# Performance work log

Hardware: AMD Instinct MI355X
Metric: run time of the kernel (lower is better)

The kernel has to match this reference:

```python
import jax, jax.numpy as jnp
import numpy as np

KSIZE = 7
HEAD_DIM = 64
EPS = 1e-6

def rmsnorm(x, w):
    return x * jax.lax.rsqrt(jnp.mean(x * x, axis=-1, keepdims=True) + EPS) * w

def rope2d(x):
    # Split channels: first half rotated by row position, second half by column position.
    B, H, W, C = x.shape
    half = C // 2
    q = half // 2
    inv = 1.0 / (10000.0 ** (jnp.arange(q, dtype=jnp.float32) / q))
    th_y = jnp.arange(H, dtype=jnp.float32)[:, None] * inv  # [H,q]
    th_x = jnp.arange(W, dtype=jnp.float32)[:, None] * inv  # [W,q]
    def rot(v, th):  # v: [...,q,2], th broadcastable to [...,q]
        c, s = jnp.cos(th), jnp.sin(th)
        a, b = v[..., 0], v[..., 1]
        return jnp.stack([a * c - b * s, a * s + b * c], axis=-1)
    xy = rot(x[..., :half].reshape(B, H, W, q, 2), th_y[None, :, None, :])
    xx = rot(x[..., half:].reshape(B, H, W, q, 2), th_x[None, None, :, :])
    return jnp.concatenate([xy.reshape(B, H, W, half), xx.reshape(B, H, W, half)], axis=-1)

def neighborhood_attn(x, w_qkv, w_proj, b_proj, k=KSIZE, hd=HEAD_DIM):
    # NATTEN semantics: each query attends to a k x k window; window start is
    # clamped at borders so every query sees exactly k*k keys.
    B, H, W, C = x.shape
    nh = C // hd
    qkv = x @ w_qkv                           # [B,H,W,3C]
    qv, kv, vv = jnp.split(qkv, 3, axis=-1)
    qh = qv.reshape(B, H, W, nh, hd)
    kh = kv.reshape(B, H, W, nh, hd)
    vh = vv.reshape(B, H, W, nh, hd)
    idx_h = jnp.clip(jnp.arange(H) - k // 2, 0, H - k)[:, None] + jnp.arange(k)  # [H,k]
    idx_w = jnp.clip(jnp.arange(W) - k // 2, 0, W - k)[:, None] + jnp.arange(k)  # [W,k]
    def gather(t):  # [B,H,W,nh,hd] -> [B,H,W,nh,k*k,hd]
        g = t[:, idx_h]            # [B,H,k,W,nh,hd]
        g = g[:, :, :, idx_w]      # [B,H,k,W,k,nh,hd]
        return g.transpose(0, 1, 3, 5, 2, 4, 6).reshape(B, H, W, nh, k * k, hd)
    kn = gather(kh)
    vn = gather(vh)
    scale = 1.0 / np.sqrt(hd).astype(np.float32)
    logits = jnp.einsum('bxynd,bxynkd->bxynk', qh, kn) * scale
    attn = jax.nn.softmax(logits, axis=-1)
    out = jnp.einsum('bxynk,bxynkd->bxynd', attn, vn).reshape(B, H, W, C)
    return out @ w_proj + b_proj

def geglu(x, ff1_w, ff1_b, ff2_w, ff2_b):
    h = x @ ff1_w + ff1_b
    gate, value = jnp.split(h, 2, axis=-1)
    return (jax.nn.gelu(gate, approximate=False) * value) @ ff2_w + ff2_b

def setup_inputs():
    key = jax.random.key(0)
    B, H, W, C = 2, 64, 64, 256
    ks = jax.random.split(key, 8)
    g = lambda k, shape, sc: jax.random.normal(k, shape, jnp.float32) * sc
    return {
        'x': g(ks[0], (B, H, W, C), 1.0),
        'norm1_w': jnp.ones((C,), jnp.float32),
        'norm2_w': jnp.ones((C,), jnp.float32),
        'w_qkv': g(ks[1], (C, 3 * C), 0.02),
        'w_proj': g(ks[2], (C, C), 0.02),
        'b_proj': g(ks[3], (C,), 0.02),
        'ff1_w': g(ks[4], (C, 2 * C), 0.02),
        'ff1_b': g(ks[5], (2 * C,), 0.02),
        'ff2_w': g(ks[6], (C, C), 0.02),
        'ff2_b': g(ks[7], (C,), 0.02),
    }

def reference(x, norm1_w, norm2_w, w_qkv, w_proj, b_proj, ff1_w, ff1_b, ff2_w, ff2_b):
    h = rope2d(rmsnorm(x, norm1_w))
    x = x + neighborhood_attn(h, w_qkv, w_proj, b_proj)
    x = x + geglu(rmsnorm(x, norm2_w), ff1_w, ff1_b, ff2_w, ff2_b)
    return x
```

## Files before the change

kernel.cpp:

```cpp
#include <hip/hip_runtime.h>
#include <hip/hip_bf16.h>


#define ROWS 8192
typedef unsigned int uint32;
typedef unsigned short ushort16;
typedef __attribute__((ext_vector_type(8))) short short8;
typedef __attribute__((ext_vector_type(4))) float floatx4;

__device__ __forceinline__ float bf2f(__hip_bfloat16 b) { return __bfloat162float(b); }
__device__ __forceinline__ float us2f(ushort16 u) {
    return __uint_as_float(((uint32)u) << 16);
}
__device__ __forceinline__ ushort16 f2us(float f) {
    __hip_bfloat16 h = __float2bfloat16(f);
    return *(ushort16*)&h;
}
__device__ __forceinline__ float ldflag(const void* p, size_t i, int f32) {
    return f32 ? ((const float*)p)[i] : bf2f(((const __hip_bfloat16*)p)[i]);
}

__device__ __forceinline__ void gl_lds16(const void* gptr, void* lptr) {
    __builtin_amdgcn_global_load_lds(
        (const __attribute__((address_space(1))) uint32*)gptr,
        (__attribute__((address_space(3))) uint32*)lptr, 16, 0, 0);
}

__global__ __launch_bounds__(64) void detect_kernel(const ushort16* __restrict__ xu,
                                                    int* __restrict__ flag) {
    const int lane = threadIdx.x;
    const float v = us2f(xu[lane * 62]);
    const float a = fabsf(v);
    const bool sane = (a < 1e4f) && (a > 1e-8f);
    const unsigned long long m = __ballot(sane);
    if (lane == 0) flag[0] = (__popcll(m) < 32) ? 1 : 0;
}

struct WSrc {
    const void *wqkv, *wproj, *ff1w, *ff2w, *bproj, *ff1b, *ff2b;
};
__global__ __launch_bounds__(256) void cvt_kernel(WSrc s, ushort16* __restrict__ wT,
                                                  float* __restrict__ bF,
                                                  const int* __restrict__ flag) {
    const int f32 = flag[0];
    const int bid = blockIdx.x, tid = threadIdx.x;
    if (bid == 112) {
        #pragma unroll
        for (int it = 0; it < 4; ++it) {
            const int j = it * 256 + tid;
            float v;
            if (j < 256)      v = ldflag(s.bproj, j, f32);
            else if (j < 768) v = ldflag(s.ff1b, j - 256, f32);
            else              v = ldflag(s.ff2b, j - 768, f32);
            bF[j] = v;
        }
        return;
    }
    const void* src; int N, kt, nt, base;
    if (bid < 48)      { src = s.wqkv;  N = 768; kt = bid / 12;      nt = bid % 12;      base = 0; }
    else if (bid < 64) { const int l = bid - 48; src = s.wproj; N = 256; kt = l / 4; nt = l % 4; base = 196608; }
    else if (bid < 96) { const int l = bid - 64; src = s.ff1w;  N = 512; kt = l / 8; nt = l % 8; base = 262144; }
    else               { const int l = bid - 96; src = s.ff2w;  N = 256; kt = l / 4; nt = l % 4; base = 393216; }

    __shared__ ushort16 T[64][65];
    const int r0 = tid >> 6, c = tid & 63;
    #pragma unroll
    for (int j = 0; j < 16; ++j) {
        const int r = j * 4 + r0;
        T[r][c] = f2us(ldflag(src, (size_t)(kt * 64 + r) * N + nt * 64 + c, f32));
    }
    __syncthreads();
    const int n = tid >> 2, kg = tid & 3;
    #pragma unroll
    for (int j = 0; j < 16; ++j) {
        const int k = kg * 16 + j;
        wT[base + (size_t)(nt * 64 + n) * 256 + kt * 64 + k] = T[k][n];
    }
}

__global__ __launch_bounds__(256) void fused_qkv(const void* __restrict__ x,
                                                 const void* __restrict__ n1w,
                                                 const ushort16* __restrict__ wqkvT,
                                                 ushort16* __restrict__ qkv,
                                                 const int* __restrict__ flag) {
    __shared__ ushort16 Apad[32 * 264];
    __shared__ ushort16 Bs[256 * 32];

    const int f32 = flag[0];
    const int tid = threadIdx.x, lane = tid & 63, wid = tid >> 6;
    const int l15 = lane & 15, kq8 = (lane >> 4) * 8;
    const int n0 = blockIdx.x * 256, m0 = blockIdx.y * 32;
    const int nw = wid * 64;
    const int cr = lane >> 2, cc = (lane & 3) * 8;

    {
        const int row = tid >> 3, s = tid & 7;
        const int gm = m0 + row;
        float v[32];
        #pragma unroll
        for (int j = 0; j < 8; ++j) {
            const size_t off = (size_t)gm * 256 + s * 32 + j * 4;
            if (f32) {
                const float4 d = *(const float4*)((const float*)x + off);
                v[j * 4] = d.x; v[j * 4 + 1] = d.y; v[j * 4 + 2] = d.z; v[j * 4 + 3] = d.w;
            } else {
                const ushort4 d = *(const ushort4*)((const ushort16*)x + off);
                v[j * 4] = us2f(d.x); v[j * 4 + 1] = us2f(d.y);
                v[j * 4 + 2] = us2f(d.z); v[j * 4 + 3] = us2f(d.w);
            }
        }
        float sq = 0.0f;
        #pragma unroll
        for (int i = 0; i < 32; ++i) sq += v[i] * v[i];
        sq += __shfl_xor(sq, 1);
        sq += __shfl_xor(sq, 2);
        sq += __shfl_xor(sq, 4);
        const float rr = rsqrtf(sq * (1.0f / 256.0f) + 1e-6f);

        const int py = (gm >> 6) & 63, px = gm & 63;
        #pragma unroll
        for (int j = 0; j < 8; ++j) {
            const int c0 = s * 32 + j * 4;
            float nv[4];
            #pragma unroll
            for (int u = 0; u < 4; ++u)
                nv[u] = v[j * 4 + u] * rr * ldflag(n1w, c0 + u, f32);
            const float pos = (c0 < 128) ? (float)py : (float)px;
            const int j0 = (c0 & 127) >> 1;
            #pragma unroll
            for (int p = 0; p < 2; ++p) {
                const float inv = expf(-(float)(j0 + p) * (9.210340371976184f / 64.0f));
                const float th = pos * inv;
                const float cs = cosf(th), sn = sinf(th);
                const float a = nv[p * 2], b = nv[p * 2 + 1];
                nv[p * 2]     = a * cs - b * sn;
                nv[p * 2 + 1] = a * sn + b * cs;
            }
            ushort4 o;
            o.x = f2us(nv[0]); o.y = f2us(nv[1]); o.z = f2us(nv[2]); o.w = f2us(nv[3]);
            *(ushort4*)&Apad[row * 264 + c0] = o;
        }
    }
    __syncthreads();

    floatx4 acc[2][4] = {};
    for (int k0 = 0; k0 < 256; k0 += 32) {
        #pragma unroll
        for (int c = 0; c < 4; ++c) {
            const int ch = wid + c * 4;
            gl_lds16(wqkvT + (size_t)(n0 + ch * 16 + cr) * 256 + k0 + cc, Bs + ch * 512);
        }
        __syncthreads();
        short8 af[2], bf[4];
        #pragma unroll
        for (int mi = 0; mi < 2; ++mi)
            af[mi] = *(const short8*)&Apad[(mi * 16 + l15) * 264 + k0 + kq8];
        #pragma unroll
        for (int nj = 0; nj < 4; ++nj)
            bf[nj] = *(const short8*)&Bs[(nw + nj * 16 + l15) * 32 + kq8];
        #pragma unroll
        for (int mi = 0; mi < 2; ++mi)
            #pragma unroll
            for (int nj = 0; nj < 4; ++nj)
                acc[mi][nj] = __builtin_amdgcn_mfma_f32_16x16x32_bf16(af[mi], bf[nj], acc[mi][nj], 0, 0, 0);
        __syncthreads();
    }

    const int crow = (lane >> 4) * 4;
    #pragma unroll
    for (int mi = 0; mi < 2; ++mi)
        #pragma unroll
        for (int nj = 0; nj < 4; ++nj)
            #pragma unroll
            for (int r = 0; r < 4; ++r) {
                const int m = m0 + mi * 16 + crow + r;
                const int n = n0 + nw + nj * 16 + l15;
                qkv[(size_t)m * 768 + n] = f2us(acc[mi][nj][r]);
            }
}

__global__ __launch_bounds__(256) void attn_kernel(const ushort16* __restrict__ qkv,
                                                   ushort16* __restrict__ ao) {
    __shared__ ushort16 smem[40208];
    ushort16* const KS = smem;
    ushort16* const VT = smem + 12544;
    ushort16* const PL = smem + 26880;

    const int tid = threadIdx.x, lane = tid & 63, wid = tid >> 6;
    const int l15 = lane & 15, kq8 = (lane >> 4) * 8;
    const int bid = blockIdx.x;
    const int h = bid & 3;
    const int t = (bid >> 2) & 63;
    const int b = bid >> 8;
    const int ty0 = (t >> 3) * 8, tx0 = (t & 7) * 8;
    const int hby = min(max(ty0 - 3, 0), 50);
    const int hbx = min(max(tx0 - 3, 0), 50);
    const int hcol = h * 64;

    const int qpl = wid * 16 + l15;
    const int qpy = ty0 + (qpl >> 3), qpx = tx0 + (qpl & 7);
    const size_t qoff = (size_t)(b * 4096 + qpy * 64 + qpx) * 768 + hcol + kq8;
    const short8 af0 = *(const short8*)&qkv[qoff];
    const short8 af1 = *(const short8*)&qkv[qoff + 32];

    for (int it = tid; it < 3136; it += 256) {
        const bool isK = it < 1568;
        const int task = isK ? it : it - 1568;
        const int key = task >> 3, oct = task & 7;
        const int pix = b * 4096 + (hby + key / 14) * 64 + hbx + key % 14;
        const uint4 d = *(const uint4*)&qkv[(size_t)pix * 768 + (isK ? 256 : 512) + hcol + oct * 8];
        if (isK) {
            uint32* dst = (uint32*)&KS[(oct >> 2) * 6272 + key * 32 + (oct & 3) * 8];
            dst[0] = d.x; dst[1] = d.y; dst[2] = d.z; dst[3] = d.w;
        } else {
            const ushort16* s8 = (const ushort16*)&d;
            #pragma unroll
            for (int j = 0; j < 8; ++j) VT[(oct * 8 + j) * 224 + key] = s8[j];
        }
    }
    for (int it = tid; it < 1792; it += 256)
        VT[(it / 28) * 224 + 196 + (it % 28)] = 0;
    __syncthreads();

    floatx4 acc[13];
    #pragma unroll
    for (int nt = 0; nt < 13; ++nt) {
        const int krow = (nt * 16 + l15) * 32 + kq8;
        const short8 bf0 = *(const short8*)&KS[krow];
        const short8 bf1 = *(const short8*)&KS[6272 + krow];
        floatx4 a = {0.0f, 0.0f, 0.0f, 0.0f};
        a = __builtin_amdgcn_mfma_f32_16x16x32_bf16(af0, bf0, a, 0, 0, 0);
        a = __builtin_amdgcn_mfma_f32_16x16x32_bf16(af1, bf1, a, 0, 0, 0);
        acc[nt] = a;
    }

    int kyA[13], kxA[13];
    #pragma unroll
    for (int nt = 0; nt < 13; ++nt) {
        const int kidx = nt * 16 + l15;
        kyA[nt] = hby + kidx / 14;
        kxA[nt] = hbx + kidx % 14;
    }

    const int crow = (lane >> 4) * 4;
    float rs[4];
    #pragma unroll
    for (int r = 0; r < 4; ++r) {
        const int pl = wid * 16 + crow + r;
        const int py = ty0 + (pl >> 3), px = tx0 + (pl & 7);
        const int sy = min(max(py - 3, 0), 57), sx = min(max(px - 3, 0), 57);
        float lv[13];
        float mx = -1e30f;
        #pragma unroll
        for (int nt = 0; nt < 13; ++nt) {
            const int kidx = nt * 16 + l15;
            const bool valid = (kidx < 196) &&
                               ((unsigned)(kyA[nt] - sy) < 7u) &&
                               ((unsigned)(kxA[nt] - sx) < 7u);
            lv[nt] = valid ? acc[nt][r] * 0.125f : -1e30f;
            mx = fmaxf(mx, lv[nt]);
        }
        #pragma unroll
        for (int off = 1; off < 16; off <<= 1) mx = fmaxf(mx, __shfl_xor(mx, off));
        float sme = 0.0f;
        #pragma unroll
        for (int nt = 0; nt < 13; ++nt) {
            const float e = exp2f((lv[nt] - mx) * 1.4426950408889634f);
            lv[nt] = e;
            sme += e;
        }
        #pragma unroll
        for (int off = 1; off < 16; off <<= 1) sme += __shfl_xor(sme, off);
        rs[r] = 1.0f / sme;
        #pragma unroll
        for (int nt = 0; nt < 13; ++nt)
            PL[pl * 208 + nt * 16 + l15] = f2us(lv[nt]);
    }
    __syncthreads();

    floatx4 oacc[4] = {};
    #pragma unroll
    for (int kc = 0; kc < 7; ++kc) {
        const short8 af = *(const short8*)&PL[(wid * 16 + l15) * 208 + kc * 32 + kq8];
        #pragma unroll
        for (int nd = 0; nd < 4; ++nd) {
            const short8 bf = *(const short8*)&VT[(nd * 16 + l15) * 224 + kc * 32 + kq8];
            oacc[nd] = __builtin_amdgcn_mfma_f32_16x16x32_bf16(af, bf, oacc[nd], 0, 0, 0);
        }
    }
    #pragma unroll
    for (int r = 0; r < 4; ++r) {
        const int pl = wid * 16 + crow + r;
        const int py = ty0 + (pl >> 3), px = tx0 + (pl & 7);
        const size_t o = (size_t)(b * 4096 + py * 64 + px) * 256 + hcol;
        #pragma unroll
        for (int nd = 0; nd < 4; ++nd)
            ao[o + nd * 16 + l15] = f2us(oacc[nd][r] * rs[r]);
    }
}

__global__ __launch_bounds__(256) void gemm_proj_rms(const ushort16* __restrict__ A,
                                                     const ushort16* __restrict__ Bt,
                                                     const float* __restrict__ bias,
                                                     const void* __restrict__ xres,
                                                     const void* __restrict__ n2w,
                                                     float* __restrict__ x1,
                                                     ushort16* __restrict__ y,
                                                     const int* __restrict__ flag) {
    constexpr int TM = 2, TN = 4;
    __shared__ ushort16 At[32 * 32];
    __shared__ ushort16 Bs[256 * 32];
    __shared__ float red[4][32];

    const int f32 = flag[0];
    const int tid = threadIdx.x, lane = tid & 63, wid = tid >> 6;
    const int m0 = blockIdx.x * 32;
    const int nw = wid * 64;
    const int cr = lane >> 2, cc = (lane & 3) * 8;
    const int l15 = lane & 15, kq = (lane >> 4) * 8;

    floatx4 acc[TM][TN] = {};

    for (int k0 = 0; k0 < 256; k0 += 32) {
        #pragma unroll
        for (int c = 0; c < 5; ++c) {
            const int ch = wid + c * 4;
            if (ch < 18) {
                const ushort16* g;
                ushort16* l;
                if (ch < 2) {
                    g = A + (size_t)(m0 + ch * 16 + cr) * 256 + k0 + cc;
                    l = At + ch * 512;
                } else {
                    const int c2 = ch - 2;
                    g = Bt + (size_t)(c2 * 16 + cr) * 256 + k0 + cc;
                    l = Bs + c2 * 512;
                }
                gl_lds16(g, l);
            }
        }
        __syncthreads();

        short8 af[TM], bf[TN];
        #pragma unroll
        for (int mi = 0; mi < TM; ++mi)
            af[mi] = *(const short8*)&At[(mi * 16 + l15) * 32 + kq];
        #pragma unroll
        for (int nj = 0; nj < TN; ++nj)
            bf[nj] = *(const short8*)&Bs[(nw + nj * 16 + l15) * 32 + kq];
        #pragma unroll
        for (int mi = 0; mi < TM; ++mi)
            #pragma unroll
            for (int nj = 0; nj < TN; ++nj)
                acc[mi][nj] = __builtin_amdgcn_mfma_f32_16x16x32_bf16(af[mi], bf[nj], acc[mi][nj], 0, 0, 0);
        __syncthreads();
    }

    const int crow = (lane >> 4) * 4;
    float w2[TN], bsv[TN];
    #pragma unroll
    for (int nj = 0; nj < TN; ++nj) {
        const int n = nw + nj * 16 + l15;
        w2[nj] = ldflag(n2w, n, f32);
        bsv[nj] = bias[n];
    }

    float ps[TM][4] = {};
    #pragma unroll
    for (int mi = 0; mi < TM; ++mi)
        #pragma unroll
        for (int nj = 0; nj < TN; ++nj)
            #pragma unroll
            for (int r = 0; r < 4; ++r) {
                const int m = m0 + mi * 16 + crow + r;
                const int n = nw + nj * 16 + l15;
                float v = acc[mi][nj][r] + bsv[nj] + ldflag(xres, (size_t)m * 256 + n, f32);
                acc[mi][nj][r] = v;
                ps[mi][r] += v * v;
            }
    #pragma unroll
    for (int off = 1; off < 16; off <<= 1)
        #pragma unroll
        for (int mi = 0; mi < TM; ++mi)
            #pragma unroll
            for (int r = 0; r < 4; ++r) ps[mi][r] += __shfl_xor(ps[mi][r], off);
    if (l15 == 0)
        #pragma unroll
        for (int mi = 0; mi < TM; ++mi)
            #pragma unroll
            for (int r = 0; r < 4; ++r) red[wid][mi * 16 + crow + r] = ps[mi][r];
    __syncthreads();

    float rr[TM][4];
    #pragma unroll
    for (int mi = 0; mi < TM; ++mi)
        #pragma unroll
        for (int r = 0; r < 4; ++r) {
            const int row = mi * 16 + crow + r;
            const float s = red[0][row] + red[1][row] + red[2][row] + red[3][row];
            rr[mi][r] = rsqrtf(s * (1.0f / 256.0f) + 1e-6f);
        }
    #pragma unroll
    for (int mi = 0; mi < TM; ++mi)
        #pragma unroll
        for (int nj = 0; nj < TN; ++nj)
            #pragma unroll
            for (int r = 0; r < 4; ++r) {
                const int m = m0 + mi * 16 + crow + r;
                const int n = nw + nj * 16 + l15;
                const size_t oi = (size_t)m * 256 + n;
                const float v = acc[mi][nj][r];
                x1[oi] = v;
                y[oi] = f2us(v * rr[mi][r] * w2[nj]);
            }
}

__global__ __launch_bounds__(256) void fused_ffn(const ushort16* __restrict__ y,
                                                 const ushort16* __restrict__ ff1wT,
                                                 const ushort16* __restrict__ ff2wT,
                                                 const float* __restrict__ bF,
                                                 const float* __restrict__ x1,
                                                 void* __restrict__ out,
                                                 const int* __restrict__ flag) {
    __shared__ ushort16 Apad[32 * 264];
    __shared__ ushort16 Bs[512 * 32];

    const int f32 = flag[0];
    const int tid = threadIdx.x, lane = tid & 63, wid = tid >> 6;
    const int l15 = lane & 15, kq8 = (lane >> 4) * 8;
    const int m0 = blockIdx.x * 32;
    const int cr = lane >> 2, cc = (lane & 3) * 8;
    const int crow = (lane >> 4) * 4;

    {
        const int row = tid >> 3, s = tid & 7;
        #pragma unroll
        for (int j = 0; j < 4; ++j) {
            const int c = s * 32 + j * 8;
            const uint4 d = *(const uint4*)&y[(size_t)(m0 + row) * 256 + c];
            *(uint4*)&Apad[row * 264 + c] = d;
        }
    }
    __syncthreads();

    floatx4 accg[2][4] = {}, accv[2][4] = {};
    for (int k0 = 0; k0 < 256; k0 += 32) {
        #pragma unroll
        for (int c = 0; c < 8; ++c) {
            const int ch = wid + c * 4;
            gl_lds16(ff1wT + (size_t)(ch * 16 + cr) * 256 + k0 + cc, Bs + ch * 512);
        }
        __syncthreads();
        short8 af[2], bg[4], bv[4];
        #pragma unroll
        for (int mi = 0; mi < 2; ++mi)
            af[mi] = *(const short8*)&Apad[(mi * 16 + l15) * 264 + k0 + kq8];
        #pragma unroll
        for (int nj = 0; nj < 4; ++nj) {
            bg[nj] = *(const short8*)&Bs[(wid * 64 + nj * 16 + l15) * 32 + kq8];
            bv[nj] = *(const short8*)&Bs[(256 + wid * 64 + nj * 16 + l15) * 32 + kq8];
        }
        #pragma unroll
        for (int mi = 0; mi < 2; ++mi)
            #pragma unroll
            for (int nj = 0; nj < 4; ++nj) {
                accg[mi][nj] = __builtin_amdgcn_mfma_f32_16x16x32_bf16(af[mi], bg[nj], accg[mi][nj], 0, 0, 0);
                accv[mi][nj] = __builtin_amdgcn_mfma_f32_16x16x32_bf16(af[mi], bv[nj], accv[mi][nj], 0, 0, 0);
            }
        __syncthreads();
    }

    #pragma unroll
    for (int mi = 0; mi < 2; ++mi)
        #pragma unroll
        for (int nj = 0; nj < 4; ++nj) {
            const int n = wid * 64 + nj * 16 + l15;
            const float bg_ = bF[256 + n], bv_ = bF[512 + n];
            #pragma unroll
            for (int r = 0; r < 4; ++r) {
                const float gate = accg[mi][nj][r] + bg_;
                const float val = accv[mi][nj][r] + bv_;
                const float ge = 0.5f * gate * (1.0f + erff(gate * 0.70710678118654752f));
                Apad[(mi * 16 + crow + r) * 264 + n] = f2us(ge * val);
            }
        }
    __syncthreads();

    floatx4 acc2[2][4] = {};
    for (int k0 = 0; k0 < 256; k0 += 32) {
        #pragma unroll
        for (int c = 0; c < 4; ++c) {
            const int ch = wid + c * 4;
            gl_lds16(ff2wT + (size_t)(ch * 16 + cr) * 256 + k0 + cc, Bs + ch * 512);
        }
        __syncthreads();
        short8 af[2], bf[4];
        #pragma unroll
        for (int mi = 0; mi < 2; ++mi)
            af[mi] = *(const short8*)&Apad[(mi * 16 + l15) * 264 + k0 + kq8];
        #pragma unroll
        for (int nj = 0; nj < 4; ++nj)
            bf[nj] = *(const short8*)&Bs[(wid * 64 + nj * 16 + l15) * 32 + kq8];
        #pragma unroll
        for (int mi = 0; mi < 2; ++mi)
            #pragma unroll
            for (int nj = 0; nj < 4; ++nj)
                acc2[mi][nj] = __builtin_amdgcn_mfma_f32_16x16x32_bf16(af[mi], bf[nj], acc2[mi][nj], 0, 0, 0);
        __syncthreads();
    }

    #pragma unroll
    for (int mi = 0; mi < 2; ++mi)
        #pragma unroll
        for (int nj = 0; nj < 4; ++nj) {
            const int n = wid * 64 + nj * 16 + l15;
            const float bs = bF[768 + n];
            #pragma unroll
            for (int r = 0; r < 4; ++r) {
                const int m = m0 + mi * 16 + crow + r;
                const size_t oi = (size_t)m * 256 + n;
                const float v = acc2[mi][nj][r] + bs + x1[oi];
                if (f32) ((float*)out)[oi] = v;
                else     ((ushort16*)out)[oi] = f2us(v);
            }
        }
}

extern "C" void kernel_launch(void* const* d_in, const int* in_sizes, int n_in,
                              void* d_out, int out_size, void* d_ws, size_t ws_size,
                              hipStream_t stream) {
    const void* x   = d_in[0];
    const void* n1w = d_in[1];
    const void* n2w = d_in[2];
    WSrc ws_src{d_in[3], d_in[4], d_in[6], d_in[8], d_in[5], d_in[7], d_in[9]};

    char* ws = (char*)d_ws;
    int*      flag = (int*)ws;
    ushort16* wT   = (ushort16*)(ws + 4096);
    float*    bF   = (float*)(ws + 4096 + 458752 * 2);
    ushort16* y    = (ushort16*)(ws + (1 << 20));
    ushort16* qkv  = (ushort16*)(ws + (5 << 20));
    ushort16* ao   = (ushort16*)(ws + (size_t)(17 << 20));
    float*    x1   = (float*)(ws + (size_t)(21 << 20));

    ushort16* wqkvT  = wT;
    ushort16* wprojT = wT + 196608;
    ushort16* ff1wT  = wT + 262144;
    ushort16* ff2wT  = wT + 393216;

    detect_kernel<<<1, 64, 0, stream>>>((const ushort16*)x, flag);
    cvt_kernel<<<113, 256, 0, stream>>>(ws_src, wT, bF, flag);
    fused_qkv<<<dim3(3, 256), 256, 0, stream>>>(x, n1w, wqkvT, qkv, flag);
    attn_kernel<<<512, 256, 0, stream>>>(qkv, ao);
    gemm_proj_rms<<<256, 256, 0, stream>>>(ao, wprojT, bF, x, n2w, x1, y, flag);
    fused_ffn<<<256, 256, 0, stream>>>(y, ff1wT, ff2wT, bF, x1, d_out, flag);
}
```

Measured before the change: 156.2 us.

## Use RoPE LUT, fast erf GELU, and async K staging with padded attention LDS

Precomputes a cos/sin table for 2D RoPE in the weight-conversion kernel so fused_qkv loads it instead of calling expf/cosf/sinf per element. Replaces erff in the GEGLU with an Abramowitz-Stegun polynomial approximation using __expf. In the attention kernel, K tiles are staged via global_load_lds directly into an oct-major LDS layout, and the V-transpose and P buffers get padded strides to reduce bank conflicts. The erf approximation adds a small accuracy error, and the LUT adds a dependent global load.

```diff
diff --git a/kernel.cpp b/kernel.cpp
--- a/kernel.cpp
+++ b/kernel.cpp
@@ -24,6 +24,17 @@
     __builtin_amdgcn_global_load_lds(
         (const __attribute__((address_space(1))) uint32*)gptr,
         (__attribute__((address_space(3))) uint32*)lptr, 16, 0, 0);
+}
+
+__device__ __forceinline__ float gelu_f(float gate) {
+    const float z = gate * 0.70710678118654752f;
+    const float az = fabsf(z);
+    const float t1 = 1.0f / fmaf(0.3275911f, az, 1.0f);
+    const float poly = ((((1.061405429f * t1 - 1.453152027f) * t1 + 1.421413741f) * t1
+                         - 0.284496736f) * t1 + 0.254829592f) * t1;
+    float erfv = 1.0f - poly * __expf(-az * az);
+    erfv = (z < 0.0f) ? -erfv : erfv;
+    return 0.5f * gate * (1.0f + erfv);
 }
 
 __global__ __launch_bounds__(64) void detect_kernel(const ushort16* __restrict__ xu,
@@ -41,6 +52,7 @@
 };
 __global__ __launch_bounds__(256) void cvt_kernel(WSrc s, ushort16* __restrict__ wT,
                                                   float* __restrict__ bF,
+                                                  float2* __restrict__ lut,
                                                   const int* __restrict__ flag) {
     const int f32 = flag[0];
     const int bid = blockIdx.x, tid = threadIdx.x;
@@ -56,6 +68,17 @@
         }
         return;
     }
+    if (bid == 113) {
+        #pragma unroll
+        for (int it = 0; it < 16; ++it) {
+            const int idx = it * 256 + tid;
+            const int pos = idx >> 6, j = idx & 63;
+            const float inv = expf(-(float)j * (9.210340371976184f / 64.0f));
+            const float th = (float)pos * inv;
+            lut[idx] = make_float2(cosf(th), sinf(th));
+        }
+        return;
+    }
     const void* src; int N, kt, nt, base;
     if (bid < 48)      { src = s.wqkv;  N = 768; kt = bid / 12;      nt = bid % 12;      base = 0; }
     else if (bid < 64) { const int l = bid - 48; src = s.wproj; N = 256; kt = l / 4; nt = l % 4; base = 196608; }
@@ -81,6 +104,7 @@
 __global__ __launch_bounds__(256) void fused_qkv(const void* __restrict__ x,
                                                  const void* __restrict__ n1w,
                                                  const ushort16* __restrict__ wqkvT,
+                                                 const float2* __restrict__ lut,
                                                  ushort16* __restrict__ qkv,
                                                  const int* __restrict__ flag) {
     __shared__ ushort16 Apad[32 * 264];
@@ -125,16 +149,14 @@
             #pragma unroll
             for (int u = 0; u < 4; ++u)
                 nv[u] = v[j * 4 + u] * rr * ldflag(n1w, c0 + u, f32);
-            const float pos = (c0 < 128) ? (float)py : (float)px;
+            const int pos = (c0 < 128) ? py : px;
             const int j0 = (c0 & 127) >> 1;
             #pragma unroll
             for (int p = 0; p < 2; ++p) {
-                const float inv = expf(-(float)(j0 + p) * (9.210340371976184f / 64.0f));
-                const float th = pos * inv;
-                const float cs = cosf(th), sn = sinf(th);
+                const float2 cs = lut[pos * 64 + j0 + p];
                 const float a = nv[p * 2], b = nv[p * 2 + 1];
-                nv[p * 2]     = a * cs - b * sn;
-                nv[p * 2 + 1] = a * sn + b * cs;
+                nv[p * 2]     = a * cs.x - b * cs.y;
+                nv[p * 2 + 1] = a * cs.y + b * cs.x;
             }
             ushort4 o;
             o.x = f2us(nv[0]); o.y = f2us(nv[1]); o.z = f2us(nv[2]); o.w = f2us(nv[3]);
@@ -181,10 +203,10 @@
 
 __global__ __launch_bounds__(256) void attn_kernel(const ushort16* __restrict__ qkv,
                                                    ushort16* __restrict__ ao) {
-    __shared__ ushort16 smem[40208];
+    __shared__ ushort16 smem[40704];
     ushort16* const KS = smem;
-    ushort16* const VT = smem + 12544;
-    ushort16* const PL = smem + 26880;
+    ushort16* const PL = smem + 12544;
+    ushort16* const VT = smem + 26112;
 
     const int tid = threadIdx.x, lane = tid & 63, wid = tid >> 6;
     const int l15 = lane & 15, kq8 = (lane >> 4) * 8;
@@ -203,31 +225,32 @@
     const short8 af0 = *(const short8*)&qkv[qoff];
     const short8 af1 = *(const short8*)&qkv[qoff + 32];
 
-    for (int it = tid; it < 3136; it += 256) {
-        const bool isK = it < 1568;
-        const int task = isK ? it : it - 1568;
-        const int key = task >> 3, oct = task & 7;
+    for (int g0 = wid * 64; g0 < 1568; g0 += 256) {
+        const int tk = min(g0 + lane, 1567);
+        const int oct = tk / 196, key = tk - oct * 196;
         const int pix = b * 4096 + (hby + key / 14) * 64 + hbx + key % 14;
-        const uint4 d = *(const uint4*)&qkv[(size_t)pix * 768 + (isK ? 256 : 512) + hcol + oct * 8];
-        if (isK) {
-            uint32* dst = (uint32*)&KS[(oct >> 2) * 6272 + key * 32 + (oct & 3) * 8];
-            dst[0] = d.x; dst[1] = d.y; dst[2] = d.z; dst[3] = d.w;
-        } else {
-            const ushort16* s8 = (const ushort16*)&d;
-            #pragma unroll
-            for (int j = 0; j < 8; ++j) VT[(oct * 8 + j) * 224 + key] = s8[j];
-        }
-    }
-    for (int it = tid; it < 1792; it += 256)
-        VT[(it / 28) * 224 + 196 + (it % 28)] = 0;
+        gl_lds16(qkv + (size_t)pix * 768 + 256 + hcol + oct * 8, KS + g0 * 8);
+    }
+    for (int it = tid; it < 1568; it += 256) {
+        const int key = it >> 3, oct = it & 7;
+        const int pix = b * 4096 + (hby + key / 14) * 64 + hbx + key % 14;
+        const uint4 d = *(const uint4*)&qkv[(size_t)pix * 768 + 512 + hcol + oct * 8];
+        const ushort16* s8 = (const ushort16*)&d;
+        #pragma unroll
+        for (int j = 0; j < 8; ++j) VT[(oct * 8 + j) * 228 + key] = s8[j];
+    }
+    for (int it = tid; it < 2048; it += 256)
+        VT[(it >> 5) * 228 + 196 + (it & 31)] = 0;
+    PL[(tid >> 2) * 212 + 208 + (tid & 3)] = 0;
     __syncthreads();
 
     floatx4 acc[13];
+    const int octA = lane >> 4;
     #pragma unroll
     for (int nt = 0; nt < 13; ++nt) {
-        const int krow = (nt * 16 + l15) * 32 + kq8;
-        const short8 bf0 = *(const short8*)&KS[krow];
-        const short8 bf1 = *(const short8*)&KS[6272 + krow];
+        const int krow = (nt * 16 + l15) * 8;
+        const short8 bf0 = *(const short8*)&KS[octA * 1568 + krow];
+        const short8 bf1 = *(const short8*)&KS[(octA + 4) * 1568 + krow];
         floatx4 a = {0.0f, 0.0f, 0.0f, 0.0f};
         a = __builtin_amdgcn_mfma_f32_16x16x32_bf16(af0, bf0, a, 0, 0, 0);
         a = __builtin_amdgcn_mfma_f32_16x16x32_bf16(af1, bf1, a, 0, 0, 0);
@@ -274,17 +297,17 @@
         rs[r] = 1.0f / sme;
         #pragma unroll
         for (int nt = 0; nt < 13; ++nt)
-            PL[pl * 208 + nt * 16 + l15] = f2us(lv[nt]);
+            PL[pl * 212 + nt * 16 + l15] = f2us(lv[nt]);
     }
     __syncthreads();
 
     floatx4 oacc[4] = {};
     #pragma unroll
     for (int kc = 0; kc < 7; ++kc) {
-        const short8 af = *(const short8*)&PL[(wid * 16 + l15) * 208 + kc * 32 + kq8];
+        const short8 af = *(const short8*)&PL[(wid * 16 + l15) * 212 + kc * 32 + kq8];
         #pragma unroll
         for (int nd = 0; nd < 4; ++nd) {
-            const short8 bf = *(const short8*)&VT[(nd * 16 + l15) * 224 + kc * 32 + kq8];
+            const short8 bf = *(const short8*)&VT[(nd * 16 + l15) * 228 + kc * 32 + kq8];
             oacc[nd] = __builtin_amdgcn_mfma_f32_16x16x32_bf16(af, bf, oacc[nd], 0, 0, 0);
         }
     }
@@ -480,8 +503,7 @@
             for (int r = 0; r < 4; ++r) {
                 const float gate = accg[mi][nj][r] + bg_;
                 const float val = accv[mi][nj][r] + bv_;
-                const float ge = 0.5f * gate * (1.0f + erff(gate * 0.70710678118654752f));
-                Apad[(mi * 16 + crow + r) * 264 + n] = f2us(ge * val);
+                Apad[(mi * 16 + crow + r) * 264 + n] = f2us(gelu_f(gate) * val);
             }
         }
     __syncthreads();
@@ -537,7 +559,8 @@
     char* ws = (char*)d_ws;
     int*      flag = (int*)ws;
     ushort16* wT   = (ushort16*)(ws + 4096);
-    float*    bF   = (float*)(ws + 4096 + 458752 * 2);
+    float*    bF   = (float*)(ws + 921600);
+    float2*   lut  = (float2*)(ws + 925696);
     ushort16* y    = (ushort16*)(ws + (1 << 20));
     ushort16* qkv  = (ushort16*)(ws + (5 << 20));
     ushort16* ao   = (ushort16*)(ws + (size_t)(17 << 20));
@@ -549,8 +572,8 @@
     ushort16* ff2wT  = wT + 393216;
 
     detect_kernel<<<1, 64, 0, stream>>>((const ushort16*)x, flag);
-    cvt_kernel<<<113, 256, 0, stream>>>(ws_src, wT, bF, flag);
-    fused_qkv<<<dim3(3, 256), 256, 0, stream>>>(x, n1w, wqkvT, qkv, flag);
+    cvt_kernel<<<114, 256, 0, stream>>>(ws_src, wT, bF, lut, flag);
+    fused_qkv<<<dim3(3, 256), 256, 0, stream>>>(x, n1w, wqkvT, lut, qkv, flag);
     attn_kernel<<<512, 256, 0, stream>>>(qkv, ao);
     gemm_proj_rms<<<256, 256, 0, stream>>>(ao, wprojT, bF, x, n2w, x1, y, flag);
     fused_ffn<<<256, 256, 0, stream>>>(y, ff1wT, ff2wT, bF, x1, d_out, flag);
```

After: 165.4 us. 1.06x slower.
